# Optimization experiments

Hardware: AMD Instinct MI355X
Metric: run time of the kernel (lower is better)

Reference implementation:

```python
import jax, jax.numpy as jnp
import numpy as np

B, T, V, D, SLOTS = 16, 4096, 32000, 512, 256
EPS = 1e-5


def setup_inputs() -> dict:
    key = jax.random.key(0)
    ks = jax.random.split(key, 12)
    s = 0.02
    return {
        "seq": jax.random.randint(ks[0], (B, T), 0, V),
        "emb": jax.random.normal(ks[1], (V, D), jnp.float32) * s,
        "w1": jax.random.normal(ks[2], (D, 2 * D), jnp.float32) * s,
        "b1": jnp.zeros((2 * D,), jnp.float32),
        "w2": jax.random.normal(ks[3], (2 * D, D), jnp.float32) * s,
        "b2": jnp.zeros((D,), jnp.float32),
        "ln_g": jnp.ones((D,), jnp.float32),
        "ln_b": jnp.zeros((D,), jnp.float32),
        "wg": jax.random.normal(ks[4], (D,), jnp.float32) * s,
        "bg": jnp.zeros((), jnp.float32),
        "wq": jax.random.normal(ks[5], (D, D), jnp.float32) * s,
        "bq": jnp.zeros((D,), jnp.float32),
        "wo": jax.random.normal(ks[6], (D, V), jnp.float32) * s,
        "bo": jnp.zeros((V,), jnp.float32),
    }


def reference(seq, emb, w1, b1, w2, b2, ln_g, ln_b, wg, bg, wq, bq, wo, bo):
    # Encoder: embed -> residual FFN -> LayerNorm
    h0 = emb[seq]                                        # [B,T,D]
    ff = jax.nn.relu(h0 @ w1 + b1) @ w2 + b2             # [B,T,D]
    x = h0 + ff
    mu = jnp.mean(x, axis=-1, keepdims=True)
    var = jnp.mean(jnp.square(x - mu), axis=-1, keepdims=True)
    h = (x - mu) * jax.lax.rsqrt(var + EPS) * ln_g + ln_b  # [B,T,D]

    # Gate -> top-k slot selection -> gather memory
    gate = jax.nn.sigmoid(h @ wg + bg)                   # [B,T]
    topk = min(SLOTS, T)
    _, top_idx = jax.lax.top_k(gate, topk)               # [B,K]
    memory = jnp.take_along_axis(h, top_idx[:, :, None], axis=1)  # [B,K,D]

    # Single-query masked softmax attention (mask is all ones)
    query_h = h[:, -1, :]                                # [B,D]
    q = query_h @ wq + bq                                # [B,D]
    scores = jnp.einsum('bkd,bd->bk', memory, q)         # [B,K]
    mask = jnp.ones((seq.shape[0], topk), jnp.float32)
    scores = jnp.where(mask == 0, -1e9, scores)
    attn = jax.nn.softmax(scores, axis=-1)               # [B,K]
    ctx = jnp.einsum('bk,bkd->bd', attn, memory)         # [B,D]
    return ctx @ wo + bo                                 # [B,V]
```

## Files before the change

### kernel.cpp

```cpp
#include <hip/hip_runtime.h>

typedef __bf16 bf16x8 __attribute__((ext_vector_type(8)));
typedef float f32x4 __attribute__((ext_vector_type(4)));
typedef unsigned short ushort8v __attribute__((ext_vector_type(8)));

#define NB 16
#define NT 4096
#define NV 32000
#define ND 512
#define NH 1024
#define NSLOTS 256

__device__ __forceinline__ float b2f(unsigned short u) {
  unsigned int x = ((unsigned int)u) << 16;
  return __builtin_bit_cast(float, x);
}
__device__ __forceinline__ unsigned short f2b(float f) {
  unsigned int x = __builtin_bit_cast(unsigned int, f);
  unsigned int r = (x + 0x7FFFu + ((x >> 16) & 1u)) >> 16;
  return (unsigned short)r;
}

#define GLOAD_LDS16(g, l)                                                              \
  __builtin_amdgcn_global_load_lds((const __attribute__((address_space(1))) void*)(g), \
                                   (__attribute__((address_space(3))) void*)(l), 16, 0, 0)
#define BARRIER() asm volatile("s_barrier" ::: "memory")
#define VMCNT(n) asm volatile("s_waitcnt vmcnt(" #n ")" ::: "memory")

__global__ __launch_bounds__(256) void cvtwt_kernel(
    const float* __restrict__ emb, unsigned short* __restrict__ embb,
    const float* __restrict__ w1, const float* __restrict__ w2,
    unsigned short* __restrict__ w1t, unsigned short* __restrict__ w2t) {
  const int blk = blockIdx.x;
  if (blk < 8000) {
    const long base = ((long)blk * 256 + threadIdx.x) * 8;
    float4 a = *(const float4*)&emb[base];
    float4 b = *(const float4*)&emb[base + 4];
    ushort8v o;
    o[0] = f2b(a.x); o[1] = f2b(a.y); o[2] = f2b(a.z); o[3] = f2b(a.w);
    o[4] = f2b(b.x); o[5] = f2b(b.y); o[6] = f2b(b.z); o[7] = f2b(b.w);
    *(ushort8v*)&embb[base] = o;
  } else {
    const int i = (blk - 8000) * 256 + threadIdx.x;
    if (i < ND * NH) {
      const int n = i >> 9, k = i & 511;
      w1t[i] = f2b(w1[k * NH + n]);
    } else {
      const int j = i - ND * NH;
      const int n = j >> 10, k = j & 1023;
      w2t[j] = f2b(w2[k * ND + n]);
    }
  }
}

template <int KDIM, int NLD, int NBN, bool RELU>
__global__ __launch_bounds__(512, 2) void gemm256_kernel(
    const unsigned short* __restrict__ Abase, const unsigned short* __restrict__ Bt,
    const float* __restrict__ bias, unsigned short* __restrict__ Out) {
  extern __shared__ unsigned short smraw[];
  const int tid = threadIdx.x;
  const int lane = tid & 63;
  const int w = tid >> 6;
  const int wm = w >> 2;
  const int wn = w & 3;

  const int id = blockIdx.x;
  const int nwg = gridDim.x;
  const int q = nwg >> 3, r = nwg & 7;
  const int xcd = id & 7;
  const int swz = ((xcd < r) ? xcd * (q + 1) : r * (q + 1) + (xcd - r) * q) + (id >> 3);
  const int bm = swz / NBN;
  const int bn = swz % NBN;

  const int srow = tid >> 3;
  const int schunk = (tid & 7) ^ (srow & 7);
  const unsigned short* aptr[4];
  const unsigned short* bptr[4];
#pragma unroll
  for (int k = 0; k < 4; ++k) {
    const int row = k * 64 + srow;
    aptr[k] = Abase + (size_t)(bm * 256 + row) * KDIM + schunk * 8;
    bptr[k] = Bt + (size_t)(bn * 256 + row) * KDIM + schunk * 8;
  }

  const int fr = lane & 15;
  const int hi = lane >> 4;

  f32x4 acc[8][4] = {};
  bf16x8 bfr[4][2];

  auto stageA = [&](int buf, int k, int kt) {
    unsigned short* A = smraw + buf * 32768;
    GLOAD_LDS16(aptr[k] + kt * 64, &A[(k * 512 + w * 64) * 8]);
  };
  auto stageB = [&](int buf, int k, int kt) {
    unsigned short* B = smraw + buf * 32768 + 16384;
    GLOAD_LDS16(bptr[k] + kt * 64, &B[(k * 512 + w * 64) * 8]);
  };

#pragma unroll
  for (int k = 0; k < 4; ++k) stageB(0, k, 0);
#pragma unroll
  for (int k = 0; k < 4; ++k) stageA(0, k, 0);
  VMCNT(0);
  BARRIER();

#define LDFRAG(base, r_, kk) \
  __builtin_bit_cast(bf16x8, *(const ushort8v*)&(base)[(r_) * 64 + (((kk) * 4 + hi) ^ (fr & 7)) * 8])
#define MFMA_PHASE(j)                                                                   \
  __builtin_amdgcn_s_setprio(1);                                                        \
  _Pragma("unroll") for (int mm = 0; mm < 2; ++mm)                                      \
      _Pragma("unroll") for (int n = 0; n < 4; ++n)                                     \
          _Pragma("unroll") for (int kk = 0; kk < 2; ++kk)                              \
              acc[2 * (j) + mm][n] =                                                    \
                  __builtin_amdgcn_mfma_f32_16x16x32_bf16(af[mm][kk], bfr[n][kk],       \
                                                          acc[2 * (j) + mm][n], 0, 0, 0); \
  __builtin_amdgcn_s_setprio(0)

  constexpr int NKT = KDIM / 64;
  for (int t = 0; t < NKT; ++t) {
    const int cur = t & 1;
    const unsigned short* A = smraw + cur * 32768;
    const unsigned short* B = A + 16384;
    const bool hn = (t + 1 < NKT);
    const int nk = t + 1;
    bf16x8 af[2][2];
#pragma unroll
    for (int n = 0; n < 4; ++n)
#pragma unroll
      for (int kk = 0; kk < 2; ++kk) bfr[n][kk] = LDFRAG(B, wn * 64 + n * 16 + fr, kk);
#pragma unroll
    for (int mm = 0; mm < 2; ++mm)
#pragma unroll
      for (int kk = 0; kk < 2; ++kk) af[mm][kk] = LDFRAG(A, wm * 128 + mm * 16 + fr, kk);
    if (hn) { stageB(cur ^ 1, 0, nk); stageB(cur ^ 1, 1, nk); }
    BARRIER();
    MFMA_PHASE(0);
#pragma unroll
    for (int mm = 0; mm < 2; ++mm)
#pragma unroll
      for (int kk = 0; kk < 2; ++kk)
        af[mm][kk] = LDFRAG(A, wm * 128 + (2 + mm) * 16 + fr, kk);
    if (hn) {
      stageB(cur ^ 1, 2, nk); stageB(cur ^ 1, 3, nk);
      VMCNT(4);
    } else {
      VMCNT(0);
    }
    BARRIER();
    MFMA_PHASE(1);
#pragma unroll
    for (int mm = 0; mm < 2; ++mm)
#pragma unroll
      for (int kk = 0; kk < 2; ++kk)
        af[mm][kk] = LDFRAG(A, wm * 128 + (4 + mm) * 16 + fr, kk);
    if (hn) { stageA(cur ^ 1, 0, nk); stageA(cur ^ 1, 2, nk); }
    BARRIER();
    MFMA_PHASE(2);
#pragma unroll
    for (int mm = 0; mm < 2; ++mm)
#pragma unroll
      for (int kk = 0; kk < 2; ++kk)
        af[mm][kk] = LDFRAG(A, wm * 128 + (6 + mm) * 16 + fr, kk);
    if (hn) {
      stageA(cur ^ 1, 1, nk); stageA(cur ^ 1, 3, nk);
      VMCNT(2);
    }
    BARRIER();
    MFMA_PHASE(3);
  }
  __syncthreads();

  float bb[4];
#pragma unroll
  for (int n = 0; n < 4; ++n) bb[n] = bias[bn * 256 + wn * 64 + n * 16 + fr];
  unsigned short* C = smraw;
#pragma unroll
  for (int h = 0; h < 2; ++h) {
    if (h) __syncthreads();
    if (wm == h) {
#pragma unroll
      for (int m = 0; m < 8; ++m)
#pragma unroll
        for (int n = 0; n < 4; ++n)
#pragma unroll
          for (int i = 0; i < 4; ++i) {
            float v = acc[m][n][i] + bb[n];
            if constexpr (RELU) v = fmaxf(v, 0.f);
            C[(m * 16 + hi * 4 + i) * 264 + wn * 64 + n * 16 + fr] = f2b(v);
          }
    }
    __syncthreads();
#pragma unroll
    for (int it = 0; it < 8; ++it) {
      const int idx = it * 512 + tid;
      const int lrow = idx >> 5;
      const int pos = idx & 31;
      ushort8v v = *(const ushort8v*)&C[lrow * 264 + pos * 8];
      *(ushort8v*)&Out[(size_t)(bm * 256 + h * 128 + lrow) * (size_t)NLD + bn * 256 + pos * 8] = v;
    }
  }
#undef LDFRAG
#undef MFMA_PHASE
}

__global__ __launch_bounds__(256) void lnv_kernel(
    const float* __restrict__ emb, const unsigned short* __restrict__ FFv,
    unsigned short* __restrict__ Hv, const float* __restrict__ ln_g,
    const float* __restrict__ ln_b, const float* __restrict__ wg,
    const float* __restrict__ bgp, float* __restrict__ gatev,
    const int* __restrict__ seq, float* __restrict__ hlast) {
  const int lane = threadIdx.x & 63;
  const int w = threadIdx.x >> 6;
  const int v = blockIdx.x * 4 + w;
  const float* er = emb + (size_t)v * ND + lane * 8;
  ushort8v fv = *(const ushort8v*)&FFv[(size_t)v * ND + lane * 8];
  float4 e0 = *(const float4*)er, e1 = *(const float4*)(er + 4);
  float x[8] = {b2f(fv[0]) + e0.x, b2f(fv[1]) + e0.y, b2f(fv[2]) + e0.z, b2f(fv[3]) + e0.w,
                b2f(fv[4]) + e1.x, b2f(fv[5]) + e1.y, b2f(fv[6]) + e1.z, b2f(fv[7]) + e1.w};
  float s = 0.f, sq = 0.f;
#pragma unroll
  for (int j = 0; j < 8; ++j) {
    s += x[j];
    sq += x[j] * x[j];
  }
#pragma unroll
  for (int o = 32; o; o >>= 1) {
    s += __shfl_xor(s, o);
    sq += __shfl_xor(sq, o);
  }
  const float mu = s * (1.f / 512.f);
  const float var = sq * (1.f / 512.f) - mu * mu;
  const float rs = rsqrtf(var + 1e-5f);
  float gd = 0.f;
  float h[8];
  ushort8v hv;
#pragma unroll
  for (int j = 0; j < 8; ++j) {
    const int col = lane * 8 + j;
    h[j] = (x[j] - mu) * rs * ln_g[col] + ln_b[col];
    hv[j] = f2b(h[j]);
    gd += h[j] * wg[col];
  }
  *(ushort8v*)&Hv[(size_t)v * ND + lane * 8] = hv;
#pragma unroll
  for (int o = 32; o; o >>= 1) gd += __shfl_xor(gd, o);
  if (lane == 0) gatev[v] = 1.f / (1.f + expf(-(gd + bgp[0])));
  for (int b = 0; b < NB; ++b) {
    if (seq[b * NT + NT - 1] == v) {
      float* hl = hlast + b * ND + lane * 8;
#pragma unroll
      for (int j = 0; j < 8; ++j) hl[j] = h[j];
    }
  }
}

__global__ __launch_bounds__(256) void topk_qpart_kernel(
    const float* __restrict__ gatev, const int* __restrict__ seq,
    int* __restrict__ topidx, const float* __restrict__ hlast,
    const float* __restrict__ wq, const float* __restrict__ bq,
    float* __restrict__ qpart) {
  __shared__ int wsum[2][4];
  __shared__ unsigned int scanbuf[256];
  const int tid = threadIdx.x;
  if (blockIdx.x >= 16) {
    const int blk = blockIdx.x - 16;
    const int b = blk >> 3, s = blk & 7;
    const int d0 = s * 64;
    float a0 = 0.f, a1 = 0.f;
#pragma unroll 4
    for (int dd = 0; dd < 64; ++dd) {
      const float hv = hlast[b * ND + d0 + dd];
      a0 += hv * wq[(size_t)(d0 + dd) * ND + tid];
      a1 += hv * wq[(size_t)(d0 + dd) * ND + tid + 256];
    }
    if (s == 0) {
      a0 += bq[tid];
      a1 += bq[tid + 256];
    }
    float* qp = qpart + ((size_t)b * 8 + s) * ND;
    qp[tid] = a0;
    qp[tid + 256] = a1;
    return;
  }
  const int b = blockIdx.x;
  const int wv = tid >> 6;
  const int lane = tid & 63;
  const int* sq_ = seq + (size_t)b * NT;
  const int base = tid * 16;
  unsigned int kreg[16];
#pragma unroll
  for (int j = 0; j < 16; ++j)
    kreg[j] = __builtin_bit_cast(unsigned int, gatev[sq_[base + j]]);

  unsigned int K = 0u;
  for (int bit = 31; bit >= 0; --bit) {
    const unsigned int cand = K | (1u << bit);
    int c = 0;
#pragma unroll
    for (int j = 0; j < 16; ++j) c += (kreg[j] >= cand) ? 1 : 0;
#pragma unroll
    for (int o = 32; o; o >>= 1) c += __shfl_xor(c, o);
    const int par = bit & 1;
    if (lane == 0) wsum[par][wv] = c;
    __syncthreads();
    const int tot = wsum[par][0] + wsum[par][1] + wsum[par][2] + wsum[par][3];
    if (tot >= NSLOTS) K = cand;
  }
  int gcnt = 0, ecnt = 0;
#pragma unroll
  for (int j = 0; j < 16; ++j) {
    gcnt += (kreg[j] > K) ? 1 : 0;
    ecnt += (kreg[j] == K) ? 1 : 0;
  }
  __syncthreads();
  scanbuf[tid] = ((unsigned int)gcnt << 16) | (unsigned int)ecnt;
  __syncthreads();
  for (int off = 1; off < 256; off <<= 1) {
    unsigned int v2 = (tid >= off) ? scanbuf[tid - off] : 0u;
    __syncthreads();
    scanbuf[tid] += v2;
    __syncthreads();
  }
  const unsigned int my = scanbuf[tid];
  const unsigned int tot = scanbuf[255];
  const int gi = (int)(my >> 16);
  const int ei = (int)(my & 0xFFFFu);
  const int tot_gt = (int)(tot >> 16);
  int gpos = gi - gcnt;
  int epos = tot_gt + (ei - ecnt);
  int* outp = topidx + b * NSLOTS;
#pragma unroll
  for (int j = 0; j < 16; ++j) {
    if (kreg[j] > K) {
      outp[gpos++] = base + j;
    } else if (kreg[j] == K) {
      if (epos < NSLOTS) outp[epos] = base + j;
      epos++;
    }
  }
}

__global__ __launch_bounds__(256) void attn_kernel(
    const unsigned short* __restrict__ Hv, const int* __restrict__ seq,
    const float* __restrict__ qpart, const int* __restrict__ topidx,
    float* __restrict__ ctx) {
  __shared__ float qs[512];
  __shared__ float attnv[256];
  __shared__ int idxs[256];
  __shared__ float red[4];
  __shared__ float part[2][128];
  const int blk = blockIdx.x;
  const int b = blk >> 2, dc = blk & 3;
  const int tid = threadIdx.x;
  const int lane = tid & 63, wv = tid >> 6;
  {
    float a0 = 0.f, a1 = 0.f;
#pragma unroll
    for (int s = 0; s < 8; ++s) {
      const float* qp = qpart + ((size_t)b * 8 + s) * ND;
      a0 += qp[tid];
      a1 += qp[tid + 256];
    }
    qs[tid] = a0;
    qs[tid + 256] = a1;
  }
  idxs[tid] = seq[(size_t)b * NT + topidx[b * 256 + tid]];
  __syncthreads();
  const unsigned short* hr = Hv + (size_t)idxs[tid] * ND;
  float sc = 0.f;
  for (int d0 = 0; d0 < 512; d0 += 8) {
    ushort8v hv = *(const ushort8v*)&hr[d0];
#pragma unroll
    for (int j = 0; j < 8; ++j) sc += b2f(hv[j]) * qs[d0 + j];
  }
  float m = sc;
#pragma unroll
  for (int o = 32; o; o >>= 1) m = fmaxf(m, __shfl_xor(m, o));
  if (lane == 0) red[wv] = m;
  __syncthreads();
  m = fmaxf(fmaxf(red[0], red[1]), fmaxf(red[2], red[3]));
  __syncthreads();
  const float e = expf(sc - m);
  float ssum = e;
#pragma unroll
  for (int o = 32; o; o >>= 1) ssum += __shfl_xor(ssum, o);
  if (lane == 0) red[wv] = ssum;
  __syncthreads();
  ssum = red[0] + red[1] + red[2] + red[3];
  attnv[tid] = e / ssum;
  __syncthreads();
  const int d = dc * 128 + (tid & 127);
  const int kh = tid >> 7;
  float c = 0.f;
#pragma unroll 4
  for (int k2 = 0; k2 < 128; ++k2) {
    const int k = kh * 128 + k2;
    c += attnv[k] * b2f(Hv[(size_t)idxs[k] * ND + d]);
  }
  part[kh][tid & 127] = c;
  __syncthreads();
  if (tid < 128) ctx[b * 512 + dc * 128 + tid] = part[0][tid] + part[1][tid];
}

__global__ __launch_bounds__(256) void out_part_kernel(const float* __restrict__ ctx,
                                                       const float* __restrict__ wo,
                                                       float* __restrict__ part) {
  const int blk = blockIdx.x;
  const int ct = blk % 125, s = blk / 125;
  const int v = ct * 256 + threadIdx.x;
  const int d0 = s * 64;
  const float* wp = wo + (size_t)d0 * NV + v;
  float acc[16] = {};
#pragma unroll 4
  for (int dd = 0; dd < 64; ++dd) {
    const float wv = wp[(size_t)dd * NV];
#pragma unroll
    for (int bb = 0; bb < 16; ++bb) acc[bb] += ctx[bb * ND + d0 + dd] * wv;
  }
  float* pp = part + (size_t)s * NB * NV + v;
#pragma unroll
  for (int bb = 0; bb < 16; ++bb) pp[(size_t)bb * NV] = acc[bb];
}

__global__ __launch_bounds__(256) void out_reduce_kernel(const float* __restrict__ part,
                                                         const float* __restrict__ bo,
                                                         float* __restrict__ out) {
  const int i = blockIdx.x * 256 + threadIdx.x;
  const int b = i / NV;
  const int v = i - b * NV;
  float a = bo[v];
#pragma unroll
  for (int s = 0; s < 8; ++s) a += part[(size_t)s * NB * NV + i];
  out[i] = a;
}

extern "C" void kernel_launch(void* const* d_in, const int* in_sizes, int n_in,
                              void* d_out, int out_size, void* d_ws, size_t ws_size,
                              hipStream_t stream) {
  const int* seq = (const int*)d_in[0];
  const float* emb = (const float*)d_in[1];
  const float* w1 = (const float*)d_in[2];
  const float* b1 = (const float*)d_in[3];
  const float* w2 = (const float*)d_in[4];
  const float* b2 = (const float*)d_in[5];
  const float* ln_g = (const float*)d_in[6];
  const float* ln_b = (const float*)d_in[7];
  const float* wg = (const float*)d_in[8];
  const float* bg = (const float*)d_in[9];
  const float* wq = (const float*)d_in[10];
  const float* bq = (const float*)d_in[11];
  const float* wo = (const float*)d_in[12];
  const float* bo = (const float*)d_in[13];
  float* out = (float*)d_out;

  char* ws = (char*)d_ws;
  unsigned short* A1v = (unsigned short*)ws;
  unsigned short* FFv = (unsigned short*)(ws + ((size_t)64 << 20));
  unsigned short* embb = (unsigned short*)(ws + ((size_t)96 << 20));
  unsigned short* Hv = (unsigned short*)(ws + ((size_t)128 << 20));
  float* part = (float*)(ws + ((size_t)160 << 20));
  unsigned short* w1t = (unsigned short*)(ws + ((size_t)177 << 20));
  unsigned short* w2t = (unsigned short*)(ws + ((size_t)178 << 20));
  char* sb = ws + ((size_t)180 << 20);
  float* gatev = (float*)sb;
  int* topidx = (int*)(sb + 131072);
  float* hlast = (float*)(sb + 131072 + 16384);
  float* ctxbuf = (float*)(sb + 131072 + 16384 + 32768);
  float* qpart = (float*)(sb + 131072 + 16384 + 65536);

  hipFuncSetAttribute(reinterpret_cast<const void*>(gemm256_kernel<512, 1024, 4, true>),
                      hipFuncAttributeMaxDynamicSharedMemorySize, 131072);
  hipFuncSetAttribute(reinterpret_cast<const void*>(gemm256_kernel<1024, 512, 2, false>),
                      hipFuncAttributeMaxDynamicSharedMemorySize, 131072);

  cvtwt_kernel<<<12096, 256, 0, stream>>>(emb, embb, w1, w2, w1t, w2t);
  gemm256_kernel<512, 1024, 4, true>
      <<<500, 512, 131072, stream>>>(embb, w1t, b1, A1v);
  gemm256_kernel<1024, 512, 2, false>
      <<<250, 512, 131072, stream>>>(A1v, w2t, b2, FFv);
  lnv_kernel<<<8000, 256, 0, stream>>>(emb, FFv, Hv, ln_g, ln_b, wg, bg, gatev, seq, hlast);
  topk_qpart_kernel<<<144, 256, 0, stream>>>(gatev, seq, topidx, hlast, wq, bq, qpart);
  attn_kernel<<<64, 256, 0, stream>>>(Hv, seq, qpart, topidx, ctxbuf);
  out_part_kernel<<<1000, 256, 0, stream>>>(ctxbuf, wo, part);
  out_reduce_kernel<<<2000, 256, 0, stream>>>(part, bo, out);
}
```

Before: 196.3 us.

## Replace 256x256 GEMM tiles with 128x128 tiles and triple-buffered K=32 pipeline

Both FFN GEMMs (over the 32000-row vocabulary-embedding table) now use 128x128 output tiles with 256 threads, K-steps of 32 and a three-stage LDS ring buffer in static shared memory, in place of 256x256 tiles with 512 threads and double-buffered K=64 steps. This quadruples the workgroup count to spread work more evenly over CUs and cuts LDS use per block, so more blocks can be resident. The trade-off is less operand reuse per tile, more global/L2 traffic, and more barriers per unit of work. The XCD swizzle is simplified to assume the grid divides evenly by 8.

```diff
diff --git a/kernel.cpp b/kernel.cpp
--- a/kernel.cpp
+++ b/kernel.cpp
@@ -54,154 +54,109 @@
 }
 
 template <int KDIM, int NLD, int NBN, bool RELU>
-__global__ __launch_bounds__(512, 2) void gemm256_kernel(
+__global__ __launch_bounds__(256) void gemm128_kernel(
     const unsigned short* __restrict__ Abase, const unsigned short* __restrict__ Bt,
     const float* __restrict__ bias, unsigned short* __restrict__ Out) {
-  extern __shared__ unsigned short smraw[];
+  __shared__ union {
+    unsigned short AB[3][2][128 * 32];
+    unsigned short C[128 * 136];
+  } sm;
   const int tid = threadIdx.x;
   const int lane = tid & 63;
   const int w = tid >> 6;
-  const int wm = w >> 2;
-  const int wn = w & 3;
 
   const int id = blockIdx.x;
-  const int nwg = gridDim.x;
-  const int q = nwg >> 3, r = nwg & 7;
-  const int xcd = id & 7;
-  const int swz = ((xcd < r) ? xcd * (q + 1) : r * (q + 1) + (xcd - r) * q) + (id >> 3);
+  const int swz = (id & 7) * (gridDim.x >> 3) + (id >> 3);
   const int bm = swz / NBN;
   const int bn = swz % NBN;
 
-  const int srow = tid >> 3;
-  const int schunk = (tid & 7) ^ (srow & 7);
-  const unsigned short* aptr[4];
-  const unsigned short* bptr[4];
-#pragma unroll
-  for (int k = 0; k < 4; ++k) {
-    const int row = k * 64 + srow;
-    aptr[k] = Abase + (size_t)(bm * 256 + row) * KDIM + schunk * 8;
-    bptr[k] = Bt + (size_t)(bn * 256 + row) * KDIM + schunk * 8;
+  const int wm = w >> 1, wn = w & 1;
+
+  const int rgrp = lane >> 2;
+  const int schunk = (lane & 3) ^ ((lane >> 3) & 3);
+  const unsigned short* aptr[2];
+  const unsigned short* bptr[2];
+#pragma unroll
+  for (int r = 0; r < 2; ++r) {
+    const int grp = w * 2 + r;
+    const int arow = bm * 128 + grp * 16 + rgrp;
+    aptr[r] = Abase + (size_t)arow * (size_t)KDIM + schunk * 8;
+    const int brow = bn * 128 + grp * 16 + rgrp;
+    bptr[r] = Bt + (size_t)brow * (size_t)KDIM + schunk * 8;
   }
 
   const int fr = lane & 15;
-  const int hi = lane >> 4;
-
-  f32x4 acc[8][4] = {};
-  bf16x8 bfr[4][2];
-
-  auto stageA = [&](int buf, int k, int kt) {
-    unsigned short* A = smraw + buf * 32768;
-    GLOAD_LDS16(aptr[k] + kt * 64, &A[(k * 512 + w * 64) * 8]);
+  const int fhi = lane >> 4;
+  const int fsw = (fr >> 1) & 3;
+  const int fchunk = (fhi ^ fsw) * 8;
+  int aoff[4], boff[4];
+#pragma unroll
+  for (int m = 0; m < 4; ++m) aoff[m] = (wm * 64 + m * 16 + fr) * 32 + fchunk;
+#pragma unroll
+  for (int n = 0; n < 4; ++n) boff[n] = (wn * 64 + n * 16 + fr) * 32 + fchunk;
+
+  f32x4 acc[4][4] = {};
+
+  auto stage = [&](int buf, int kt) {
+#pragma unroll
+    for (int r = 0; r < 2; ++r) {
+      const int grp = w * 2 + r;
+      GLOAD_LDS16(aptr[r] + kt * 32, &sm.AB[buf][0][grp * 512]);
+      GLOAD_LDS16(bptr[r] + kt * 32, &sm.AB[buf][1][grp * 512]);
+    }
   };
-  auto stageB = [&](int buf, int k, int kt) {
-    unsigned short* B = smraw + buf * 32768 + 16384;
-    GLOAD_LDS16(bptr[k] + kt * 64, &B[(k * 512 + w * 64) * 8]);
-  };
-
-#pragma unroll
-  for (int k = 0; k < 4; ++k) stageB(0, k, 0);
-#pragma unroll
-  for (int k = 0; k < 4; ++k) stageA(0, k, 0);
-  VMCNT(0);
-  BARRIER();
-
-#define LDFRAG(base, r_, kk) \
-  __builtin_bit_cast(bf16x8, *(const ushort8v*)&(base)[(r_) * 64 + (((kk) * 4 + hi) ^ (fr & 7)) * 8])
-#define MFMA_PHASE(j)                                                                   \
-  __builtin_amdgcn_s_setprio(1);                                                        \
-  _Pragma("unroll") for (int mm = 0; mm < 2; ++mm)                                      \
-      _Pragma("unroll") for (int n = 0; n < 4; ++n)                                     \
-          _Pragma("unroll") for (int kk = 0; kk < 2; ++kk)                              \
-              acc[2 * (j) + mm][n] =                                                    \
-                  __builtin_amdgcn_mfma_f32_16x16x32_bf16(af[mm][kk], bfr[n][kk],       \
-                                                          acc[2 * (j) + mm][n], 0, 0, 0); \
-  __builtin_amdgcn_s_setprio(0)
-
-  constexpr int NKT = KDIM / 64;
-  for (int t = 0; t < NKT; ++t) {
-    const int cur = t & 1;
-    const unsigned short* A = smraw + cur * 32768;
-    const unsigned short* B = A + 16384;
-    const bool hn = (t + 1 < NKT);
-    const int nk = t + 1;
-    bf16x8 af[2][2];
+
+  constexpr int NKT = KDIM / 32;
+  stage(0, 0);
+  stage(1, 1);
+  for (int kt = 0; kt < NKT; ++kt) {
+    if (kt + 1 < NKT)
+      asm volatile("s_waitcnt vmcnt(4)" ::: "memory");
+    else
+      asm volatile("s_waitcnt vmcnt(0)" ::: "memory");
+    __builtin_amdgcn_s_barrier();
+    if (kt + 2 < NKT) stage((kt + 2) % 3, kt + 2);
+    const int cur = kt % 3;
+    bf16x8 af[4], bfr[4];
+#pragma unroll
+    for (int m = 0; m < 4; ++m)
+      af[m] = __builtin_bit_cast(bf16x8, *(const ushort8v*)&sm.AB[cur][0][aoff[m]]);
 #pragma unroll
     for (int n = 0; n < 4; ++n)
-#pragma unroll
-      for (int kk = 0; kk < 2; ++kk) bfr[n][kk] = LDFRAG(B, wn * 64 + n * 16 + fr, kk);
-#pragma unroll
-    for (int mm = 0; mm < 2; ++mm)
-#pragma unroll
-      for (int kk = 0; kk < 2; ++kk) af[mm][kk] = LDFRAG(A, wm * 128 + mm * 16 + fr, kk);
-    if (hn) { stageB(cur ^ 1, 0, nk); stageB(cur ^ 1, 1, nk); }
-    BARRIER();
-    MFMA_PHASE(0);
-#pragma unroll
-    for (int mm = 0; mm < 2; ++mm)
-#pragma unroll
-      for (int kk = 0; kk < 2; ++kk)
-        af[mm][kk] = LDFRAG(A, wm * 128 + (2 + mm) * 16 + fr, kk);
-    if (hn) {
-      stageB(cur ^ 1, 2, nk); stageB(cur ^ 1, 3, nk);
-      VMCNT(4);
-    } else {
-      VMCNT(0);
-    }
-    BARRIER();
-    MFMA_PHASE(1);
-#pragma unroll
-    for (int mm = 0; mm < 2; ++mm)
-#pragma unroll
-      for (int kk = 0; kk < 2; ++kk)
-        af[mm][kk] = LDFRAG(A, wm * 128 + (4 + mm) * 16 + fr, kk);
-    if (hn) { stageA(cur ^ 1, 0, nk); stageA(cur ^ 1, 2, nk); }
-    BARRIER();
-    MFMA_PHASE(2);
-#pragma unroll
-    for (int mm = 0; mm < 2; ++mm)
-#pragma unroll
-      for (int kk = 0; kk < 2; ++kk)
-        af[mm][kk] = LDFRAG(A, wm * 128 + (6 + mm) * 16 + fr, kk);
-    if (hn) {
-      stageA(cur ^ 1, 1, nk); stageA(cur ^ 1, 3, nk);
-      VMCNT(2);
-    }
-    BARRIER();
-    MFMA_PHASE(3);
-  }
-  __syncthreads();
-
-  float bb[4];
-#pragma unroll
-  for (int n = 0; n < 4; ++n) bb[n] = bias[bn * 256 + wn * 64 + n * 16 + fr];
-  unsigned short* C = smraw;
-#pragma unroll
-  for (int h = 0; h < 2; ++h) {
-    if (h) __syncthreads();
-    if (wm == h) {
-#pragma unroll
-      for (int m = 0; m < 8; ++m)
-#pragma unroll
-        for (int n = 0; n < 4; ++n)
-#pragma unroll
-          for (int i = 0; i < 4; ++i) {
-            float v = acc[m][n][i] + bb[n];
-            if constexpr (RELU) v = fmaxf(v, 0.f);
-            C[(m * 16 + hi * 4 + i) * 264 + wn * 64 + n * 16 + fr] = f2b(v);
-          }
-    }
-    __syncthreads();
-#pragma unroll
-    for (int it = 0; it < 8; ++it) {
-      const int idx = it * 512 + tid;
-      const int lrow = idx >> 5;
-      const int pos = idx & 31;
-      ushort8v v = *(const ushort8v*)&C[lrow * 264 + pos * 8];
-      *(ushort8v*)&Out[(size_t)(bm * 256 + h * 128 + lrow) * (size_t)NLD + bn * 256 + pos * 8] = v;
-    }
-  }
-#undef LDFRAG
-#undef MFMA_PHASE
+      bfr[n] = __builtin_bit_cast(bf16x8, *(const ushort8v*)&sm.AB[cur][1][boff[n]]);
+    __builtin_amdgcn_s_setprio(1);
+#pragma unroll
+    for (int m = 0; m < 4; ++m)
+#pragma unroll
+      for (int n = 0; n < 4; ++n)
+        acc[m][n] = __builtin_amdgcn_mfma_f32_16x16x32_bf16(af[m], bfr[n], acc[m][n], 0, 0, 0);
+    __builtin_amdgcn_s_setprio(0);
+  }
+  __builtin_amdgcn_s_barrier();
+
+#pragma unroll
+  for (int m = 0; m < 4; ++m)
+#pragma unroll
+    for (int n = 0; n < 4; ++n) {
+      const int col_l = wn * 64 + n * 16 + fr;
+      const float bb = bias[bn * 128 + col_l];
+      const int row_l0 = wm * 64 + m * 16 + (fhi << 2);
+#pragma unroll
+      for (int i = 0; i < 4; ++i) {
+        float v = acc[m][n][i] + bb;
+        if constexpr (RELU) v = fmaxf(v, 0.f);
+        sm.C[(row_l0 + i) * 136 + col_l] = f2b(v);
+      }
+    }
+  __syncthreads();
+#pragma unroll
+  for (int r8 = 0; r8 < 8; ++r8) {
+    const int chunk = r8 * 256 + tid;
+    const int row = chunk >> 4;
+    const int c8 = (chunk & 15) * 8;
+    ushort8v v = *(const ushort8v*)&sm.C[row * 136 + c8];
+    *(ushort8v*)&Out[(size_t)(bm * 128 + row) * (size_t)NLD + bn * 128 + c8] = v;
+  }
 }
 
 __global__ __launch_bounds__(256) void lnv_kernel(
@@ -469,16 +424,11 @@
   float* ctxbuf = (float*)(sb + 131072 + 16384 + 32768);
   float* qpart = (float*)(sb + 131072 + 16384 + 65536);
 
-  hipFuncSetAttribute(reinterpret_cast<const void*>(gemm256_kernel<512, 1024, 4, true>),
-                      hipFuncAttributeMaxDynamicSharedMemorySize, 131072);
-  hipFuncSetAttribute(reinterpret_cast<const void*>(gemm256_kernel<1024, 512, 2, false>),
-                      hipFuncAttributeMaxDynamicSharedMemorySize, 131072);
-
   cvtwt_kernel<<<12096, 256, 0, stream>>>(emb, embb, w1, w2, w1t, w2t);
-  gemm256_kernel<512, 1024, 4, true>
-      <<<500, 512, 131072, stream>>>(embb, w1t, b1, A1v);
-  gemm256_kernel<1024, 512, 2, false>
-      <<<250, 512, 131072, stream>>>(A1v, w2t, b2, FFv);
+  gemm128_kernel<512, 1024, 8, true>
+      <<<2000, 256, 0, stream>>>(embb, w1t, b1, A1v);
+  gemm128_kernel<1024, 512, 4, false>
+      <<<1000, 256, 0, stream>>>(A1v, w2t, b2, FFv);
   lnv_kernel<<<8000, 256, 0, stream>>>(emb, FFv, Hv, ln_g, ln_b, wg, bg, gatev, seq, hlast);
   topk_qpart_kernel<<<144, 256, 0, stream>>>(gatev, seq, topidx, hlast, wq, bq, qpart);
   attn_kernel<<<64, 256, 0, stream>>>(Hv, seq, qpart, topidx, ctxbuf);
```

Result: slower. 206.3 us (+5.1%).
